# Performance work log

Hardware: AMD Instinct MI355X
Metric: run time of the kernel (lower is better)

The kernel has to match this reference:

```python
import jax, jax.numpy as jnp
import numpy as np

NEG = -1e30  # log-space 'zero' that keeps gradients finite (vs -inf)


def setup_inputs() -> dict:
    key = jax.random.key(0)
    k1, k2, k3, k4 = jax.random.split(key, 4)
    B, T, V, S = 32, 2048, 128, 256
    predictions = jax.random.normal(k1, (B, T, V), dtype=jnp.float32)
    # input lengths in [T//2, T]; target lengths in [S//4, S]; labels in [1, V) (0 is blank)
    prediction_lengths = jax.random.randint(k2, (B,), T // 2, T + 1, dtype=jnp.int32)
    ground_truths = jax.random.randint(k3, (B, S), 1, V, dtype=jnp.int32)
    ground_truth_lengths = jax.random.randint(k4, (B,), S // 4, S + 1, dtype=jnp.int32)
    return {
        "predictions": predictions,
        "prediction_lengths": prediction_lengths,
        "ground_truths": ground_truths,
        "ground_truth_lengths": ground_truth_lengths,
    }


def _ctc_loss(log_probs, targets, input_lengths, target_lengths, blank=0):
    # log_probs: [T, B, V]; targets: [B, S]
    T, B, V = log_probs.shape
    S = targets.shape[1]
    L = 2 * S + 1  # extended label sequence: blank, l1, blank, l2, ..., blank
    ext = jnp.full((B, L), blank, dtype=targets.dtype).at[:, 1::2].set(targets)
    # skip transition s-2 -> s allowed iff ext[s] != blank and ext[s] != ext[s-2]
    skip = jnp.concatenate(
        [jnp.zeros((B, 2), dtype=bool), (ext[:, 2:] != blank) & (ext[:, 2:] != ext[:, :-2])],
        axis=1,
    )
    # gather per-extended-label log-probs: [T, B, L]
    lp_ext = jnp.take_along_axis(log_probs, jnp.broadcast_to(ext[None], (T, B, L)), axis=2)

    alpha0 = (
        jnp.full((B, L), NEG, dtype=log_probs.dtype)
        .at[:, 0].set(lp_ext[0, :, 0])
        .at[:, 1].set(lp_ext[0, :, 1])
    )

    def step(alpha, lp_t):
        a1 = alpha
        a2 = jnp.pad(alpha[:, :-1], ((0, 0), (1, 0)), constant_values=NEG)
        a3 = jnp.where(skip, jnp.pad(alpha[:, :-2], ((0, 0), (2, 0)), constant_values=NEG), NEG)
        m = jnp.maximum(jnp.maximum(a1, a2), a3)
        new = m + jnp.log(jnp.exp(a1 - m) + jnp.exp(a2 - m) + jnp.exp(a3 - m)) + lp_t
        return new, new

    _, alphas = jax.lax.scan(step, alpha0, lp_ext[1:])
    alphas = jnp.concatenate([alpha0[None], alphas], axis=0)  # [T, B, L]

    bidx = jnp.arange(B)
    alpha_final = alphas[input_lengths - 1, bidx]  # [B, L] at each sequence's last frame
    last = 2 * target_lengths  # index of final blank; last-1 is final label
    loss = -jnp.logaddexp(alpha_final[bidx, last], alpha_final[bidx, last - 1])
    loss = jnp.where(loss < 1e10, loss, 0.0)  # zero_infinity=True
    # torch reduction='mean': per-sample loss / target_length, then batch mean
    return (loss / target_lengths.astype(loss.dtype)).mean()


def reference(predictions, prediction_lengths, ground_truths, ground_truth_lengths):
    # module: transpose to [T, B, V], log_softmax over vocab, then CTC loss
    log_probs = jax.nn.log_softmax(jnp.transpose(predictions, (1, 0, 2)), axis=2)
    return _ctc_loss(log_probs, ground_truths, prediction_lengths, ground_truth_lengths, blank=0)
```

## Files before the change

### kernel.cpp

```cpp
#include <hip/hip_runtime.h>
#include <math.h>

constexpr int V = 128;

__device__ __forceinline__ double dpp_shr1_f64(double x) {
    int lo = __builtin_amdgcn_update_dpp(0, __double2loint(x), 0x138, 0xf, 0xf, false);
    int hi = __builtin_amdgcn_update_dpp(0, __double2hiint(x), 0x138, 0xf, 0xf, false);
    return __hiloint2double(hi, lo);
}
__device__ __forceinline__ double dpp_shl1_f64(double x) {
    int lo = __builtin_amdgcn_update_dpp(0, __double2loint(x), 0x130, 0xf, 0xf, false);
    int hi = __builtin_amdgcn_update_dpp(0, __double2hiint(x), 0x130, 0xf, 0xf, false);
    return __hiloint2double(hi, lo);
}

__device__ __forceinline__ unsigned f32_to_bf16_rne(float f) {
    unsigned u = __float_as_uint(f);
    return (u + 0x7fffu + ((u >> 16) & 1u)) >> 16;
}

__global__ __launch_bounds__(256) void ctc_prelude(
    const float* __restrict__ pred, const int* __restrict__ gt,
    const int* __restrict__ gt_len, const int* __restrict__ pred_len,
    char* __restrict__ g16, float* __restrict__ z, int* __restrict__ flags,
    int T, int S)
{
    if (blockIdx.x == 0 && threadIdx.x < 65) flags[threadIdx.x] = 0;

    int wid  = blockIdx.x * 4 + (threadIdx.x >> 6);
    int lane = threadIdx.x & 63;
    int w4   = threadIdx.x >> 6;
    int b    = wid / T;
    int t    = wid - b * T;
    if (t >= pred_len[b]) return;
    __shared__ float rows[4][V];

    const float2* p = (const float2*)pred + (size_t)wid * 64;
    float2 v = p[lane];
    rows[w4][2 * lane]     = v.x;
    rows[w4][2 * lane + 1] = v.y;
    float x0 = __shfl(v.x, 0, 64);
    float s = __expf(v.x) + __expf(v.y);
    #pragma unroll
    for (int off = 32; off >= 1; off >>= 1) s += __shfl_xor(s, off, 64);
    if (lane == 0) z[wid] = __logf(s) - v.x;

    int4 la = *(const int4*)(gt + b * S + 4 * lane);
    int tl = gt_len[b];
    float4 o;
    o.x = (4 * lane + 0 < tl) ? __expf(rows[w4][la.x] - x0) : 0.f;
    o.y = (4 * lane + 1 < tl) ? __expf(rows[w4][la.y] - x0) : 0.f;
    o.z = (4 * lane + 2 < tl) ? __expf(rows[w4][la.z] - x0) : 0.f;
    o.w = (4 * lane + 3 < tl) ? __expf(rows[w4][la.w] - x0) : 0.f;

    uint2 w;
    w.x = f32_to_bf16_rne(o.x) | (f32_to_bf16_rne(o.y) << 16);
    w.y = f32_to_bf16_rne(o.z) | (f32_to_bf16_rne(o.w) << 16);
    *(uint2*)(g16 + (size_t)wid * 512 + lane * 8) = w;
}

__global__ __launch_bounds__(128, 1) void ctc_scan_bi(
    const char*  __restrict__ g16,
    const int*   __restrict__ pred_len,
    const int*   __restrict__ gt,
    const int*   __restrict__ gt_len,
    const float* __restrict__ z,
    double*      __restrict__ fwdv,
    double*      __restrict__ bwdv,
    int*         __restrict__ Kf,
    int*         __restrict__ Kb,
    int* done, int* gdone, float* lossb,
    float* __restrict__ out,
    int T, int S, int B)
{
    const int blk  = blockIdx.x;
    const int b    = blk >> 1;
    const int dir  = blk & 1;
    const int wv   = threadIdx.x >> 6;
    const int lane = threadIdx.x & 63;
    const int len  = pred_len[b];
    const int tl   = gt_len[b];
    const int L    = 2 * tl + 1;
    const int m    = (len + 1) >> 1;

    __shared__ uint2 ring[2][32][64];

    int4 la = *(const int4*)(gt + b * S + 4 * lane);
    int law_up = __shfl_up(la.w, 1, 64);
    int lax_dn = __shfl_down(la.x, 1, 64);
    const double sk0 = (lane > 0 && la.x != law_up) ? 1.0 : 0.0;
    const double sk1 = (la.y != la.x) ? 1.0 : 0.0;
    const double sk2 = (la.z != la.y) ? 1.0 : 0.0;
    const double sk3 = (la.w != la.z) ? 1.0 : 0.0;
    const double sk4 = (lax_dn != la.w) ? 1.0 : 0.0;

    const char* gb = g16 + (size_t)b * T * 512 + lane * 8;

    double u[9];
    int K = 0;

    auto RESCALE = [&]() {
        double mx = u[0];
        #pragma unroll
        for (int j = 1; j < 9; ++j) mx = fmax(mx, u[j]);
        #pragma unroll
        for (int off = 32; off >= 1; off >>= 1)
            mx = fmax(mx, __shfl_xor(mx, off, 64));
        int k = ((__double2hiint(mx) >> 20) & 0x7ff) - 1023;
        #pragma unroll
        for (int j = 0; j < 9; ++j) u[j] = ldexp(u[j], -k);
        K += k;
    };

    auto FSTEP_Q = [&](uint2 q) {
        double um1 = dpp_shr1_f64(u[7]);
        double gx = (double)__uint_as_float(q.x << 16);
        double gy = (double)__uint_as_float(q.x & 0xffff0000u);
        double gz = (double)__uint_as_float(q.y << 16);
        double gw = (double)__uint_as_float(q.y & 0xffff0000u);
        u[8] = u[8] + u[7];
        u[7] = (fma(sk3, u[5], u[6]) + u[7]) * gw;
        u[6] = u[6] + u[5];
        u[5] = (fma(sk2, u[3], u[4]) + u[5]) * gz;
        u[4] = u[4] + u[3];
        u[3] = (fma(sk1, u[1], u[2]) + u[3]) * gy;
        u[2] = u[2] + u[1];
        u[1] = (fma(sk0, um1, u[0]) + u[1]) * gx;
        u[0] = u[0] + um1;
    };

    auto BSTEP_Q = [&](uint2 q) {
        double d0 = dpp_shl1_f64(u[0]);
        if (lane == 63) d0 = u[8];
        double gx = (double)__uint_as_float(q.x << 16);
        double gy = (double)__uint_as_float(q.x & 0xffff0000u);
        double gz = (double)__uint_as_float(q.y << 16);
        double gw = (double)__uint_as_float(q.y & 0xffff0000u);
        double p1 = gx * u[1], p3 = gy * u[3];
        double p5 = gz * u[5], p7 = gw * u[7];
        double dp = dpp_shl1_f64(p1);
        u[0] = u[0] + p1;
        u[1] = fma(sk1, p3, u[2]) + p1;
        u[2] = u[2] + p3;
        u[3] = fma(sk2, p5, u[4]) + p3;
        u[4] = u[4] + p5;
        u[5] = fma(sk3, p7, u[6]) + p5;
        u[6] = u[6] + p7;
        u[7] = fma(sk4, dp, d0) + p7;
    };

    auto PRODUCE = [&](int buf, int r0, int stride ) {
        uint2 tmp[16];
        #pragma unroll
        for (int j = 0; j < 16; ++j)
            tmp[j] = *(const uint2*)(gb + (size_t)(r0 + stride * j) * 512);
        #pragma unroll
        for (int j = 0; j < 16; ++j) ring[buf][j][lane] = tmp[j];
        #pragma unroll
        for (int j = 0; j < 16; ++j)
            tmp[j] = *(const uint2*)(gb + (size_t)(r0 + stride * (16 + j)) * 512);
        #pragma unroll
        for (int j = 0; j < 16; ++j) ring[buf][16 + j][lane] = tmp[j];
    };

    if (dir == 0) {
        #pragma unroll
        for (int j = 0; j < 9; ++j) u[j] = 0.0;
        const int nrows = m;
        const int nch = (nrows + 31) >> 5;
        for (int it = 0; it <= nch; ++it) {
            if (wv == 1 && it < nch)
                PRODUCE(it & 1, it << 5, +1);
            if (wv == 0 && it >= 1) {
                int c = it - 1;
                int buf = c & 1;
                uint2 rr[4];
                #pragma unroll
                for (int j = 0; j < 4; ++j) rr[j] = ring[buf][j][lane];
                if (c == 0) {
                    if (lane == 0) {
                        u[0] = 1.0;
                        u[1] = (double)__uint_as_float(rr[0].x << 16);
                    }
                    rr[0] = ring[buf][4][lane];
                    #pragma unroll
                    for (int i = 1; i < 32; ++i) {
                        uint2 q = rr[i & 3];
                        if (i + 4 < 32) rr[i & 3] = ring[buf][i + 4][lane];
                        FSTEP_Q(q);
                    }
                } else if (((c + 1) << 5) <= nrows) {
                    #pragma unroll
                    for (int i = 0; i < 32; ++i) {
                        uint2 q = rr[i & 3];
                        if (i + 4 < 32) rr[i & 3] = ring[buf][i + 4][lane];
                        FSTEP_Q(q);
                    }
                } else {
                    int rem = nrows - (c << 5);
                    #pragma unroll
                    for (int i = 0; i < 32; ++i) {
                        if (i < rem) {
                            uint2 q = rr[i & 3];
                            if (i + 4 < 32) rr[i & 3] = ring[buf][i + 4][lane];
                            FSTEP_Q(q);
                        }
                    }
                }
                if (c & 1) RESCALE();
            }
            __syncthreads();
        }
        if (wv == 0) {
            RESCALE();
            double* outv = fwdv + (size_t)b * 520;
            #pragma unroll
            for (int j = 0; j < 8; ++j) outv[8 * lane + j] = u[j];
            if (lane == 63) outv[512] = u[8];
            if (lane == 0)  Kf[b] = K;
        }
    } else {
        const int nb = len - m;
        #pragma unroll
        for (int j = 0; j < 8; ++j) {
            int s = 8 * lane + j;
            u[j] = (s == 2 * tl || s == 2 * tl - 1) ? 1.0 : 0.0;
        }
        u[8] = (lane == 63 && L == 513) ? 1.0 : 0.0;
        const int nrows = nb;
        const int nch = (nrows + 31) >> 5;
        for (int it = 0; it <= nch; ++it) {
            if (wv == 1 && it < nch)
                PRODUCE(it & 1, len - 1 - (it << 5), -1);
            if (wv == 0 && it >= 1) {
                int c = it - 1;
                int buf = c & 1;
                uint2 rr[4];
                #pragma unroll
                for (int j = 0; j < 4; ++j) rr[j] = ring[buf][j][lane];
                if (((c + 1) << 5) <= nrows) {
                    #pragma unroll
                    for (int i = 0; i < 32; ++i) {
                        uint2 q = rr[i & 3];
                        if (i + 4 < 32) rr[i & 3] = ring[buf][i + 4][lane];
                        BSTEP_Q(q);
                    }
                } else {
                    int rem = nrows - (c << 5);
                    #pragma unroll
                    for (int i = 0; i < 32; ++i) {
                        if (i < rem) {
                            uint2 q = rr[i & 3];
                            if (i + 4 < 32) rr[i & 3] = ring[buf][i + 4][lane];
                            BSTEP_Q(q);
                        }
                    }
                }
                if (c & 1) RESCALE();
            }
            __syncthreads();
        }
        if (wv == 0) {
            RESCALE();
            double* outv = bwdv + (size_t)b * 520;
            #pragma unroll
            for (int j = 0; j < 8; ++j) outv[8 * lane + j] = u[j];
            if (lane == 63) outv[512] = u[8];
            if (lane == 0)  Kb[b] = K;
        }
    }

    if (wv != 0) return;

    __threadfence();
    int prev = 0;
    if (lane == 0)
        prev = __hip_atomic_fetch_add(&done[b], 1, __ATOMIC_ACQ_REL,
                                      __HIP_MEMORY_SCOPE_AGENT);
    prev = __shfl(prev, 0, 64);
    if (prev == 0) return;
    __threadfence();

    const double* f = fwdv + (size_t)b * 520;
    const double* w = bwdv + (size_t)b * 520;
    double c = 0.0;
    #pragma unroll
    for (int j = 0; j < 8; ++j)
        c = fma(f[8 * lane + j], w[8 * lane + j], c);
    if (lane == 63) c = fma(f[512], w[512], c);
    #pragma unroll
    for (int off = 32; off >= 1; off >>= 1) c += __shfl_xor(c, off, 64);

    double zs = 0.0;
    const float* zb = z + b * T;
    int t = lane;
    for (; t + 448 < len; t += 512) {
        float a0 = zb[t],       a1 = zb[t + 64],  a2 = zb[t + 128];
        float a3 = zb[t + 192], a4 = zb[t + 256], a5 = zb[t + 320];
        float a6 = zb[t + 384], a7 = zb[t + 448];
        zs += (((double)a0 + a1) + ((double)a2 + a3))
            + (((double)a4 + a5) + ((double)a6 + a7));
    }
    for (; t < len; t += 64) zs += (double)zb[t];
    #pragma unroll
    for (int off = 32; off >= 1; off >>= 1) zs += __shfl_xor(zs, off, 64);

    if (lane == 0) {
        double logp = log(c)
                    + (double)(Kf[b] + Kb[b]) * 0.6931471805599453 - zs;
        double loss = -logp;
        if (!(loss < 1e10)) loss = 0.0;
        if (loss < 0.0)     loss = 0.0;
        lossb[b] = (float)(loss / (double)tl);
        __threadfence();
        int pg = __hip_atomic_fetch_add(gdone, 1, __ATOMIC_ACQ_REL,
                                        __HIP_MEMORY_SCOPE_AGENT);
        if (pg == B - 1) {
            __threadfence();
            float ssum = 0.0f;
            for (int i = 0; i < B; ++i) ssum += lossb[i];
            out[0] = ssum / (float)B;
        }
    }
}

constexpr int SPL  = 9;
constexpr int RING = 32;

__global__ void ctc_reduce_kernel(const float* __restrict__ ls,
                                  float* __restrict__ out, int B)
{
    if (blockIdx.x == 0 && threadIdx.x == 0) {
        float s = 0.0f;
        for (int i = 0; i < B; ++i) s += ls[i];
        out[0] = s / (float)B;
    }
}

__global__ __launch_bounds__(256) void softmax_z_kernel(
    const float* __restrict__ pred, float* __restrict__ z, int nrows)
{
    int w    = blockIdx.x * 4 + (threadIdx.x >> 6);
    int lane = threadIdx.x & 63;
    if (w >= nrows) return;
    const float2* p = (const float2*)pred;
    float2 v = p[(size_t)w * 64 + lane];
    float s = __expf(v.x) + __expf(v.y);
    #pragma unroll
    for (int off = 32; off >= 1; off >>= 1) s += __shfl_xor(s, off, 64);
    if (lane == 0) z[w] = __logf(s);
}

__device__ __forceinline__ void ctc_step_fb(
    const float* __restrict__ rowbase, const int* __restrict__ goff,
    const double* __restrict__ skd, double (&u)[SPL], int lane)
{
    float gf[SPL];
    #pragma unroll
    for (int j = 0; j < SPL; ++j)
        gf[j] = *(const float*)((const char*)rowbase + goff[j]);
    double um1 = __shfl_up(u[8], 1, 64);
    double um2 = __shfl_up(u[7], 1, 64);
    if (lane == 0) { um1 = 0.0; um2 = 0.0; }
    #pragma unroll
    for (int jj = 0; jj < SPL; ++jj) {
        int j = SPL - 1 - jj;
        double a2 = (j >= 1) ? u[j - 1] : um1;
        double a3 = (j >= 2) ? u[j - 2] : ((j == 1) ? um1 : um2);
        double t  = fma(skd[j], a3, a2) + u[j];
        u[j] = t * (double)gf[j];
    }
}

__device__ __forceinline__ void ctc_rescale_fb(double (&u)[SPL], int& K)
{
    double m = u[0];
    #pragma unroll
    for (int j = 1; j < SPL; ++j) m = fmax(m, u[j]);
    #pragma unroll
    for (int off = 32; off >= 1; off >>= 1) m = fmax(m, __shfl_xor(m, off, 64));
    if (m > 0.0) {
        int e = (__double2hiint(m) >> 20) & 0x7ff;
        int k = e - 1023;
        #pragma unroll
        for (int j = 0; j < SPL; ++j) u[j] = ldexp(u[j], -k);
        K += k;
    }
}

__global__ __launch_bounds__(64) void ctc_scan_kernel(
    const float* __restrict__ pred, const int* __restrict__ pred_len,
    const int* __restrict__ gt, const int* __restrict__ gt_len,
    const float* __restrict__ z, float* __restrict__ loss_out, int T, int S)
{
    const int b    = blockIdx.x;
    const int lane = threadIdx.x;
    const int len  = pred_len[b];
    const int tl   = gt_len[b];
    const int L    = 2 * tl + 1;

    __shared__ float ring[RING][V];
    __shared__ int   gts[512];

    for (int i = lane; i < S; i += 64) gts[i] = gt[b * S + i];
    __syncthreads();

    int    goff[SPL];
    double skd[SPL];
    #pragma unroll
    for (int j = 0; j < SPL; ++j) {
        int s = SPL * lane + j;
        int e = 0, ep = 0;
        if (s < L && (s & 1)) e = gts[s >> 1];
        if (s >= 2 && s < L && (s & 1)) ep = gts[(s - 2) >> 1];
        goff[j] = e * 4;
        skd[j]  = (s >= 2 && s < L && e != 0 && e != ep) ? 1.0 : 0.0;
    }

    const float2* rowp = (const float2*)(pred + (size_t)b * T * V);
    float2 raw[16];

    #pragma unroll
    for (int i = 0; i < 16; ++i) raw[i] = rowp[(size_t)i * 64 + lane];
    #pragma unroll
    for (int i = 0; i < 16; ++i) {
        float2 w; w.x = __expf(raw[i].x); w.y = __expf(raw[i].y);
        *(float2*)&ring[i][2 * lane] = w;
    }
    #pragma unroll
    for (int i = 0; i < 16; ++i) raw[i] = rowp[(size_t)(16 + i) * 64 + lane];
    #pragma unroll
    for (int i = 0; i < 16; ++i) {
        float2 w; w.x = __expf(raw[i].x); w.y = __expf(raw[i].y);
        *(float2*)&ring[16 + i][2 * lane] = w;
    }
    #pragma unroll
    for (int i = 0; i < 16; ++i) {
        int r = 32 + i; if (r > T - 1) r = T - 1;
        raw[i] = rowp[(size_t)r * 64 + lane];
    }

    double u[SPL];
    #pragma unroll
    for (int j = 0; j < SPL; ++j) {
        int s = SPL * lane + j;
        float w0 = *(const float*)((const char*)&ring[0][0] + goff[j]);
        u[j] = (s < 2) ? (double)w0 : 0.0;
    }
    int K = 0;

    for (int t = 1; t < 16 && t < len; ++t)
        ctc_step_fb(&ring[t & (RING - 1)][0], goff, skd, u, lane);
    ctc_rescale_fb(u, K);

    int tb = 16;
    for (; tb + 16 <= len; tb += 16) {
        #pragma unroll
        for (int i = 0; i < 16; ++i) {
            float2 w; w.x = __expf(raw[i].x); w.y = __expf(raw[i].y);
            *(float2*)&ring[(tb + 16 + i) & (RING - 1)][2 * lane] = w;
        }
        #pragma unroll
        for (int i = 0; i < 16; ++i) {
            int r = tb + 32 + i; if (r > T - 1) r = T - 1;
            raw[i] = rowp[(size_t)r * 64 + lane];
        }
        #pragma unroll
        for (int i = 0; i < 16; ++i)
            ctc_step_fb(&ring[(tb + i) & (RING - 1)][0], goff, skd, u, lane);
        ctc_rescale_fb(u, K);
    }

    for (int t = tb; t < len; ++t)
        ctc_step_fb(&ring[t & (RING - 1)][0], goff, skd, u, lane);

    double contrib = 0.0;
    #pragma unroll
    for (int j = 0; j < SPL; ++j) {
        int s = SPL * lane + j;
        if (s == L - 1 || s == L - 2) contrib += u[j];
    }
    #pragma unroll
    for (int off = 32; off >= 1; off >>= 1)
        contrib += __shfl_xor(contrib, off, 64);

    double zsum = 0.0;
    for (int t = lane; t < len; t += 64) zsum += (double)z[b * T + t];
    #pragma unroll
    for (int off = 32; off >= 1; off >>= 1)
        zsum += __shfl_xor(zsum, off, 64);

    if (lane == 0) {
        double lg    = log(contrib);
        double alpha = lg + (double)K * 0.6931471805599453 - zsum;
        double loss  = -alpha;
        if (!(loss < 1e10)) loss = 0.0;
        loss_out[b] = (float)(loss / (double)tl);
    }
}

extern "C" void kernel_launch(void* const* d_in, const int* in_sizes, int n_in,
                              void* d_out, int out_size, void* d_ws, size_t ws_size,
                              hipStream_t stream) {
    const float* pred = (const float*)d_in[0];
    const int*   plen = (const int*)d_in[1];
    const int*   gts  = (const int*)d_in[2];
    const int*   glen = (const int*)d_in[3];

    const int B = in_sizes[1];
    const int S = in_sizes[2] / B;
    const int T = in_sizes[0] / (B * V);
    const size_t BT = (size_t)B * T;

    float* out = (float*)d_out;
    char*  ws  = (char*)d_ws;

    size_t off_fl  = 0;
    size_t off_z   = 1024;
    size_t off_fw  = (off_z + BT * 4 + 255) & ~(size_t)255;
    size_t off_bw  = off_fw  + (size_t)B * 520 * 8;
    size_t off_kf  = off_bw  + (size_t)B * 520 * 8;
    size_t off_kb  = off_kf  + (size_t)B * 4;
    size_t off_g   = (off_kb + (size_t)B * 4 + 1023) & ~(size_t)1023;
    size_t need    = off_g + BT * 512;

    bool fast_ok = (ws_size >= need) && (S == 256) && (T % 4 == 0) &&
                   (T >= 128) && (B >= 1) && (B <= 64);

    if (fast_ok) {
        int*    flags = (int*)(ws + off_fl);
        int*    done  = flags;
        int*    gdone = flags + 64;
        float*  lossb = (float*)(ws + off_fl + 512);
        float*  zp    = (float*)(ws + off_z);
        double* fw    = (double*)(ws + off_fw);
        double* bw    = (double*)(ws + off_bw);
        int*    kf    = (int*)(ws + off_kf);
        int*    kb    = (int*)(ws + off_kb);
        char*   g16   = ws + off_g;

        ctc_prelude<<<B * T / 4, 256, 0, stream>>>(pred, gts, glen, plen,
                                                   g16, zp, flags, T, S);
        ctc_scan_bi<<<2 * B, 128, 0, stream>>>(g16, plen, gts, glen, zp,
                                               fw, bw, kf, kb,
                                               done, gdone, lossb, out, T, S, B);
    } else {
        float* zbuf = (float*)ws;
        float* lb   = zbuf + BT;
        int nrows = B * T;
        softmax_z_kernel<<<(nrows + 3) / 4, 256, 0, stream>>>(pred, zbuf, nrows);
        ctc_scan_kernel<<<B, 64, 0, stream>>>(pred, plen, gts, glen, zbuf, lb, T, S);
        ctc_reduce_kernel<<<1, 64, 0, stream>>>(lb, out, B);
    }
}
```

Measured before the change: 167.9 us.

## Fuse softmax prelude into bidirectional CTC scan with producer and logsumexp waves

```diff
diff --git a/kernel.cpp b/kernel.cpp
--- a/kernel.cpp
+++ b/kernel.cpp
@@ -19,56 +19,16 @@
     return (u + 0x7fffu + ((u >> 16) & 1u)) >> 16;
 }
 
-__global__ __launch_bounds__(256) void ctc_prelude(
-    const float* __restrict__ pred, const int* __restrict__ gt,
-    const int* __restrict__ gt_len, const int* __restrict__ pred_len,
-    char* __restrict__ g16, float* __restrict__ z, int* __restrict__ flags,
-    int T, int S)
-{
-    if (blockIdx.x == 0 && threadIdx.x < 65) flags[threadIdx.x] = 0;
-
-    int wid  = blockIdx.x * 4 + (threadIdx.x >> 6);
-    int lane = threadIdx.x & 63;
-    int w4   = threadIdx.x >> 6;
-    int b    = wid / T;
-    int t    = wid - b * T;
-    if (t >= pred_len[b]) return;
-    __shared__ float rows[4][V];
-
-    const float2* p = (const float2*)pred + (size_t)wid * 64;
-    float2 v = p[lane];
-    rows[w4][2 * lane]     = v.x;
-    rows[w4][2 * lane + 1] = v.y;
-    float x0 = __shfl(v.x, 0, 64);
-    float s = __expf(v.x) + __expf(v.y);
-    #pragma unroll
-    for (int off = 32; off >= 1; off >>= 1) s += __shfl_xor(s, off, 64);
-    if (lane == 0) z[wid] = __logf(s) - v.x;
-
-    int4 la = *(const int4*)(gt + b * S + 4 * lane);
-    int tl = gt_len[b];
-    float4 o;
-    o.x = (4 * lane + 0 < tl) ? __expf(rows[w4][la.x] - x0) : 0.f;
-    o.y = (4 * lane + 1 < tl) ? __expf(rows[w4][la.y] - x0) : 0.f;
-    o.z = (4 * lane + 2 < tl) ? __expf(rows[w4][la.z] - x0) : 0.f;
-    o.w = (4 * lane + 3 < tl) ? __expf(rows[w4][la.w] - x0) : 0.f;
-
-    uint2 w;
-    w.x = f32_to_bf16_rne(o.x) | (f32_to_bf16_rne(o.y) << 16);
-    w.y = f32_to_bf16_rne(o.z) | (f32_to_bf16_rne(o.w) << 16);
-    *(uint2*)(g16 + (size_t)wid * 512 + lane * 8) = w;
-}
-
-__global__ __launch_bounds__(128, 1) void ctc_scan_bi(
-    const char*  __restrict__ g16,
+__global__ __launch_bounds__(192, 1) void ctc_fused_bi(
+    const float* __restrict__ pred,
     const int*   __restrict__ pred_len,
     const int*   __restrict__ gt,
     const int*   __restrict__ gt_len,
-    const float* __restrict__ z,
     double*      __restrict__ fwdv,
     double*      __restrict__ bwdv,
     int*         __restrict__ Kf,
     int*         __restrict__ Kb,
+    double*      __restrict__ zpart,
     int* done, int* gdone, float* lossb,
     float* __restrict__ out,
     int T, int S, int B)
@@ -83,7 +43,8 @@
     const int L    = 2 * tl + 1;
     const int m    = (len + 1) >> 1;
 
-    __shared__ uint2 ring[2][32][64];
+    __shared__ uint2  ring[2][32][64];
+    __shared__ double zsh;
 
     int4 la = *(const int4*)(gt + b * S + 4 * lane);
     int law_up = __shfl_up(la.w, 1, 64);
@@ -94,10 +55,11 @@
     const double sk3 = (la.w != la.z) ? 1.0 : 0.0;
     const double sk4 = (lax_dn != la.w) ? 1.0 : 0.0;
 
-    const char* gb = g16 + (size_t)b * T * 512 + lane * 8;
+    const float2* rowp = (const float2*)(pred + (size_t)b * T * V);
 
     double u[9];
-    int K = 0;
+    int    K  = 0;
+    double zs = 0.0;
 
     auto RESCALE = [&]() {
         double mx = u[0];
@@ -149,18 +111,32 @@
         u[7] = fma(sk4, dp, d0) + p7;
     };
 
-    auto PRODUCE = [&](int buf, int r0, int stride ) {
-        uint2 tmp[16];
-        #pragma unroll
-        for (int j = 0; j < 16; ++j)
-            tmp[j] = *(const uint2*)(gb + (size_t)(r0 + stride * j) * 512);
-        #pragma unroll
-        for (int j = 0; j < 16; ++j) ring[buf][j][lane] = tmp[j];
-        #pragma unroll
-        for (int j = 0; j < 16; ++j)
-            tmp[j] = *(const uint2*)(gb + (size_t)(r0 + stride * (16 + j)) * 512);
-        #pragma unroll
-        for (int j = 0; j < 16; ++j) ring[buf][16 + j][lane] = tmp[j];
+    auto GROW = [&](float2 v, int buf, int idx) {
+        float x0 = __shfl(v.x, 0, 64);
+        float a0 = __shfl(v.x, la.x >> 1, 64), b0 = __shfl(v.y, la.x >> 1, 64);
+        float a1 = __shfl(v.x, la.y >> 1, 64), b1 = __shfl(v.y, la.y >> 1, 64);
+        float a2 = __shfl(v.x, la.z >> 1, 64), b2 = __shfl(v.y, la.z >> 1, 64);
+        float a3 = __shfl(v.x, la.w >> 1, 64), b3 = __shfl(v.y, la.w >> 1, 64);
+        float g0 = (la.x & 1) ? b0 : a0;
+        float g1 = (la.y & 1) ? b1 : a1;
+        float g2 = (la.z & 1) ? b2 : a2;
+        float g3 = (la.w & 1) ? b3 : a3;
+        float o0 = (4 * lane + 0 < tl) ? __expf(g0 - x0) : 0.f;
+        float o1 = (4 * lane + 1 < tl) ? __expf(g1 - x0) : 0.f;
+        float o2 = (4 * lane + 2 < tl) ? __expf(g2 - x0) : 0.f;
+        float o3 = (4 * lane + 3 < tl) ? __expf(g3 - x0) : 0.f;
+        uint2 w;
+        w.x = f32_to_bf16_rne(o0) | (f32_to_bf16_rne(o1) << 16);
+        w.y = f32_to_bf16_rne(o2) | (f32_to_bf16_rne(o3) << 16);
+        ring[buf][idx][lane] = w;
+    };
+
+    auto ZROW = [&](float2 v, bool keep) {
+        float x0 = __shfl(v.x, 0, 64);
+        float s = __expf(v.x - x0) + __expf(v.y - x0);
+        #pragma unroll
+        for (int off = 32; off >= 1; off >>= 1) s += __shfl_xor(s, off, 64);
+        if (keep) zs += (double)__logf(s);
     };
 
     if (dir == 0) {
@@ -169,8 +145,31 @@
         const int nrows = m;
         const int nch = (nrows + 31) >> 5;
         for (int it = 0; it <= nch; ++it) {
-            if (wv == 1 && it < nch)
-                PRODUCE(it & 1, it << 5, +1);
+            if (wv == 1 && it < nch) {
+                int base = it << 5, buf = it & 1;
+                #pragma unroll
+                for (int h = 0; h < 2; ++h) {
+                    float2 vr[16];
+                    #pragma unroll
+                    for (int j = 0; j < 16; ++j)
+                        vr[j] = rowp[(size_t)(base + h * 16 + j) * 64 + lane];
+                    #pragma unroll
+                    for (int j = 0; j < 16; ++j) GROW(vr[j], buf, h * 16 + j);
+                }
+            }
+            if (wv == 2 && it < nch) {
+                int base = it << 5;
+                #pragma unroll
+                for (int h = 0; h < 2; ++h) {
+                    float2 vr[16];
+                    #pragma unroll
+                    for (int j = 0; j < 16; ++j)
+                        vr[j] = rowp[(size_t)(base + h * 16 + j) * 64 + lane];
+                    #pragma unroll
+                    for (int j = 0; j < 16; ++j)
+                        ZROW(vr[j], base + h * 16 + j < nrows);
+                }
+            }
             if (wv == 0 && it >= 1) {
                 int c = it - 1;
                 int buf = c & 1;
@@ -230,8 +229,31 @@
         const int nrows = nb;
         const int nch = (nrows + 31) >> 5;
         for (int it = 0; it <= nch; ++it) {
-            if (wv == 1 && it < nch)
-                PRODUCE(it & 1, len - 1 - (it << 5), -1);
+            if (wv == 1 && it < nch) {
+                int base = it << 5, buf = it & 1;
+                #pragma unroll
+                for (int h = 0; h < 2; ++h) {
+                    float2 vr[16];
+                    #pragma unroll
+                    for (int j = 0; j < 16; ++j)
+                        vr[j] = rowp[(size_t)(len - 1 - (base + h * 16 + j)) * 64 + lane];
+                    #pragma unroll
+                    for (int j = 0; j < 16; ++j) GROW(vr[j], buf, h * 16 + j);
+                }
+            }
+            if (wv == 2 && it < nch) {
+                int base = it << 5;
+                #pragma unroll
+                for (int h = 0; h < 2; ++h) {
+                    float2 vr[16];
+                    #pragma unroll
+                    for (int j = 0; j < 16; ++j)
+                        vr[j] = rowp[(size_t)(len - 1 - (base + h * 16 + j)) * 64 + lane];
+                    #pragma unroll
+                    for (int j = 0; j < 16; ++j)
+                        ZROW(vr[j], base + h * 16 + j < nrows);
+                }
+            }
             if (wv == 0 && it >= 1) {
                 int c = it - 1;
                 int buf = c & 1;
@@ -270,8 +292,11 @@
         }
     }
 
+    if (wv == 2 && lane == 0) zsh = zs;
+    __syncthreads();
     if (wv != 0) return;
 
+    if (lane == 0) zpart[blk] = zsh;
     __threadfence();
     int prev = 0;
     if (lane == 0)
@@ -291,23 +316,10 @@
     #pragma unroll
     for (int off = 32; off >= 1; off >>= 1) c += __shfl_xor(c, off, 64);
 
-    double zs = 0.0;
-    const float* zb = z + b * T;
-    int t = lane;
-    for (; t + 448 < len; t += 512) {
-        float a0 = zb[t],       a1 = zb[t + 64],  a2 = zb[t + 128];
-        float a3 = zb[t + 192], a4 = zb[t + 256], a5 = zb[t + 320];
-        float a6 = zb[t + 384], a7 = zb[t + 448];
-        zs += (((double)a0 + a1) + ((double)a2 + a3))
-            + (((double)a4 + a5) + ((double)a6 + a7));
-    }
-    for (; t < len; t += 64) zs += (double)zb[t];
-    #pragma unroll
-    for (int off = 32; off >= 1; off >>= 1) zs += __shfl_xor(zs, off, 64);
-
     if (lane == 0) {
+        double zstot = zpart[2 * b] + zpart[2 * b + 1];
         double logp = log(c)
-                    + (double)(Kf[b] + Kb[b]) * 0.6931471805599453 - zs;
+                    + (double)(Kf[b] + Kb[b]) * 0.6931471805599453 - zstot;
         double loss = -logp;
         if (!(loss < 1e10)) loss = 0.0;
         if (loss < 0.0)     loss = 0.0;
@@ -515,16 +527,15 @@
     float* out = (float*)d_out;
     char*  ws  = (char*)d_ws;
 
-    size_t off_fl  = 0;
-    size_t off_z   = 1024;
-    size_t off_fw  = (off_z + BT * 4 + 255) & ~(size_t)255;
-    size_t off_bw  = off_fw  + (size_t)B * 520 * 8;
-    size_t off_kf  = off_bw  + (size_t)B * 520 * 8;
-    size_t off_kb  = off_kf  + (size_t)B * 4;
-    size_t off_g   = (off_kb + (size_t)B * 4 + 1023) & ~(size_t)1023;
-    size_t need    = off_g + BT * 512;
-
-    bool fast_ok = (ws_size >= need) && (S == 256) && (T % 4 == 0) &&
+    size_t off_fl = 0;
+    size_t off_zp = 1024;
+    size_t off_fw = 2048;
+    size_t off_bw = off_fw + (size_t)B * 520 * 8;
+    size_t off_kf = off_bw + (size_t)B * 520 * 8;
+    size_t off_kb = off_kf + (size_t)B * 4;
+    size_t need   = off_kb + (size_t)B * 4;
+
+    bool fast_ok = (ws_size >= need) && (S == 256) &&
                    (T >= 128) && (B >= 1) && (B <= 64);
 
     if (fast_ok) {
@@ -532,18 +543,17 @@
         int*    done  = flags;
         int*    gdone = flags + 64;
         float*  lossb = (float*)(ws + off_fl + 512);
-        float*  zp    = (float*)(ws + off_z);
+        double* zp    = (double*)(ws + off_zp);
         double* fw    = (double*)(ws + off_fw);
         double* bw    = (double*)(ws + off_bw);
         int*    kf    = (int*)(ws + off_kf);
         int*    kb    = (int*)(ws + off_kb);
-        char*   g16   = ws + off_g;
-
-        ctc_prelude<<<B * T / 4, 256, 0, stream>>>(pred, gts, glen, plen,
-                                                   g16, zp, flags, T, S);
-        ctc_scan_bi<<<2 * B, 128, 0, stream>>>(g16, plen, gts, glen, zp,
-                                               fw, bw, kf, kb,
-                                               done, gdone, lossb, out, T, S, B);
+
+        hipMemsetAsync(ws + off_fl, 0, 512, stream);
+        ctc_fused_bi<<<2 * B, 192, 0, stream>>>(pred, plen, gts, glen,
+                                                fw, bw, kf, kb, zp,
+                                                done, gdone, lossb, out,
+                                                T, S, B);
     } else {
         float* zbuf = (float*)ws;
         float* lb   = zbuf + BT;
```

New measurement: 284.0 us. 69.1% more time.
